# Kernel tuning notes

Measured on AMD Instinct MI355X. Metric: run time of the kernel, lower is better.

Reference implementation:

```python
import jax, jax.numpy as jnp
import numpy as np

N = 512
H = 128
L = 4
NUM_RBF = 50
CUTOFF = 5.0
NMOL = 16
OUT = 1


def setup_inputs() -> dict:
    key = jax.random.key(0)
    ks = jax.random.split(key, 12)
    s = lambda f: 1.0 / np.sqrt(f)
    atomic_numbers = jax.random.randint(ks[0], (N,), 0, 100)
    positions = jax.random.normal(ks[1], (N, 3), dtype=jnp.float32) * 2.0
    batch = jnp.sort(jax.random.randint(ks[2], (N,), 0, NMOL))
    return {
        'atomic_numbers': atomic_numbers,
        'positions': positions,
        'batch': batch,
        'embed': jax.random.normal(ks[3], (100, H), dtype=jnp.float32) * 0.1,
        'msg_w1': jax.random.normal(ks[4], (L, H + NUM_RBF + 3, H), dtype=jnp.float32) * s(H + NUM_RBF + 3),
        'msg_b1': jnp.zeros((L, H), jnp.float32),
        'msg_w2': jax.random.normal(ks[5], (L, H, H), dtype=jnp.float32) * s(H),
        'msg_b2': jnp.zeros((L, H), jnp.float32),
        'upd_w1': jax.random.normal(ks[6], (L, 2 * H, H), dtype=jnp.float32) * s(2 * H),
        'upd_b1': jnp.zeros((L, H), jnp.float32),
        'upd_w2': jax.random.normal(ks[7], (L, H, H), dtype=jnp.float32) * s(H),
        'upd_b2': jnp.zeros((L, H), jnp.float32),
        'out_w1': jax.random.normal(ks[8], (H, H // 2), dtype=jnp.float32) * s(H),
        'out_b1': jnp.zeros((H // 2,), jnp.float32),
        'out_w2': jax.random.normal(ks[9], (H // 2, OUT), dtype=jnp.float32) * s(H // 2),
        'out_b2': jnp.zeros((OUT,), jnp.float32),
    }


def _forward(atomic_numbers, positions, batch, embed, msg_w1, msg_b1, msg_w2,
             msg_b2, upd_w1, upd_b1, upd_w2, upd_b2, out_w1, out_b1, out_w2, out_b2):
    x = embed[jnp.clip(atomic_numbers, 0, 99)]                      # [N,H]
    # all-pairs geometry: row i = source, col j = target (matches repeat_interleave/repeat)
    diff = positions[:, None, :] - positions[None, :, :]            # [N,N,3]
    dist = jnp.linalg.norm(diff, axis=-1)                           # [N,N]
    not_self = jnp.arange(N)[:, None] != jnp.arange(N)[None, :]
    valid = (dist < CUTOFF) & not_self                              # [N,N] edge mask
    dirs = diff / jnp.maximum(dist, 1e-8)[..., None]                # [N,N,3]
    # gaussian RBF: centers linspace(0, cutoff, num_rbf), width = cutoff/num_rbf
    centers = jnp.linspace(0.0, CUTOFF, NUM_RBF)
    width = CUTOFF / NUM_RBF
    rbf = jnp.exp(-(dist[..., None] - centers) ** 2 / (2.0 * width ** 2))  # [N,N,50]

    for l in range(L):
        # Linear over concat([x_j, rbf, dirs]) split by input blocks (same math)
        Wx = msg_w1[l, :H]
        Wr = msg_w1[l, H:H + NUM_RBF]
        Wd = msg_w1[l, H + NUM_RBF:]
        pre = (x @ Wx)[:, None, :] \
            + jnp.einsum('ijr,rh->ijh', rbf, Wr) \
            + jnp.einsum('ijd,dh->ijh', dirs, Wd) + msg_b1[l]       # [N,N,H]
        m = jax.nn.silu(pre) @ msg_w2[l] + msg_b2[l]                # [N,N,H]
        m = jnp.where(valid[..., None], m, 0.0)
        aggr = m.sum(axis=0)                                        # scatter-add to target j
        upd_in = jnp.concatenate([x, aggr], axis=-1)                # [N,2H]
        x = x + jax.nn.silu(upd_in @ upd_w1[l] + upd_b1[l]) @ upd_w2[l] + upd_b2[l]

    # per-molecule mean pool
    sums = jax.ops.segment_sum(x, batch, num_segments=NMOL)         # [NMOL,H]
    counts = jax.ops.segment_sum(jnp.ones((N,), x.dtype), batch, num_segments=NMOL)
    pooled = sums / jnp.maximum(counts, 1.0)[:, None]
    return jax.nn.silu(pooled @ out_w1 + out_b1) @ out_w2 + out_b2  # [NMOL,OUT]


def reference(atomic_numbers, positions, batch, embed, msg_w1, msg_b1, msg_w2,
              msg_b2, upd_w1, upd_b1, upd_w2, upd_b2, out_w1, out_b1, out_w2, out_b2):
    return _forward(atomic_numbers, positions, batch, embed, msg_w1, msg_b1, msg_w2,
                    msg_b2, upd_w1, upd_b1, upd_w2, upd_b2, out_w1, out_b1, out_w2, out_b2)
```

## Files before the change

### kernel.cpp

```cpp
#include <hip/hip_runtime.h>
#include <math.h>

#define N 512
#define H 128
#define L 4
#define NUM_RBF 50
#define NMOL 16
#define SUPER 64
#define FSTRIDE 72

typedef __attribute__((ext_vector_type(8))) short short8;
typedef __attribute__((ext_vector_type(4))) float float4v;
typedef __attribute__((ext_vector_type(4))) int int4v;

__device__ __forceinline__ float silu_f(float v) {
    return v / (1.0f + __expf(-v));
}

__device__ __forceinline__ unsigned short f2bf(float f) {
    unsigned int u = __float_as_uint(f);
    unsigned int r = (u + 0x7FFFu + ((u >> 16) & 1u)) >> 16;
    return (unsigned short)r;
}

__global__ __launch_bounds__(512) void k_embed_lin(const int* __restrict__ an,
                                                   const float* __restrict__ embed,
                                                   const float* __restrict__ pos,
                                                   const float* __restrict__ wx,
                                                   const float* __restrict__ b1,
                                                   float* __restrict__ x,
                                                   float* __restrict__ a,
                                                   int* __restrict__ nbr,
                                                   int* __restrict__ ncnt) {
    int j = blockIdx.x;
    int tid = threadIdx.x;
    int lane = tid & 63;
    int wave = tid >> 6;
    int h = tid & 127;
    int grp = tid >> 7;

    __shared__ float xs[H];
    __shared__ int wsum8[8];
    __shared__ float part[4][H];

    float pjx = pos[j * 3 + 0], pjy = pos[j * 3 + 1], pjz = pos[j * 3 + 2];

    if (tid < H) {
        int z = an[j];
        z = min(max(z, 0), 99);
        float xv = embed[z * H + tid];
        xs[tid] = xv;
        x[j * H + tid] = xv;
    }

    {
        int i = tid;
        float dx = pos[i * 3 + 0] - pjx;
        float dy = pos[i * 3 + 1] - pjy;
        float dz = pos[i * 3 + 2] - pjz;
        float d2 = dx * dx + dy * dy + dz * dz;
        int valid = (d2 < 25.0f) && (i != j);
        unsigned long long m = __ballot(valid);
        int pre = __popcll(m & ((1ull << lane) - 1ull));
        if (lane == 0) wsum8[wave] = __popcll(m);
        __syncthreads();
        int wbase = 0, total = 0;
        for (int w = 0; w < 8; w++) {
            if (w < wave) wbase += wsum8[w];
            total += wsum8[w];
        }
        if (valid) nbr[j * 512 + wbase + pre] = i;
        int padded = (total + 63) & ~63;
        for (int s = total + tid; s < padded; s += 512) nbr[j * 512 + s] = j;
        if (tid == 0) ncnt[j] = total;
    }

    {
        float p0 = 0.f, p1 = 0.f, p2 = 0.f, p3 = 0.f;
        int k0 = grp * 32;
#pragma unroll 8
        for (int k = 0; k < 32; k += 4) {
            p0 += xs[k0 + k]     * wx[(k0 + k)     * H + h];
            p1 += xs[k0 + k + 1] * wx[(k0 + k + 1) * H + h];
            p2 += xs[k0 + k + 2] * wx[(k0 + k + 2) * H + h];
            p3 += xs[k0 + k + 3] * wx[(k0 + k + 3) * H + h];
        }
        part[grp][h] = (p0 + p1) + (p2 + p3);
    }
    __syncthreads();
    if (grp == 0)
        a[j * H + h] = part[0][h] + part[1][h] + part[2][h] + part[3][h] + b1[h];
}

__global__ __launch_bounds__(512) void k_layer(const float* __restrict__ a,
                                               const float* __restrict__ pos,
                                               const int* __restrict__ nbr,
                                               const int* __restrict__ ncnt,
                                               const float* __restrict__ wfeat,
                                               const float* __restrict__ w2,
                                               const float* __restrict__ b2,
                                               const float* __restrict__ u1,
                                               const float* __restrict__ ub1,
                                               const float* __restrict__ u2,
                                               const float* __restrict__ ub2,
                                               float* __restrict__ x,
                                               const float* __restrict__ wxn,
                                               const float* __restrict__ b1n,
                                               float* __restrict__ a_next) {
    int j = blockIdx.x;
    int tid = threadIdx.x;
    int g = tid >> 8;
    int t8 = tid & 255;
    int lane = tid & 63;
    int wv4 = (tid >> 6) & 3;
    int nn = lane & 15;
    int quad = lane >> 4;
    int hbase = wv4 * 32;

    __shared__ unsigned short F[2][2][SUPER * FSTRIDE];
    __shared__ int nidx[2][2][SUPER];
    __shared__ float sjp[2][H];
    __shared__ float sj[H], xj[H], ag[H], hid[H], xn[H];
    __shared__ float part[4][H];

    int cnt = ncnt[j];
    float pjx = pos[j * 3 + 0], pjy = pos[j * 3 + 1], pjz = pos[j * 3 + 2];

    if (tid < 2 * H) sjp[tid >> 7][tid & 127] = 0.0f;
    if (tid < H) xj[tid] = x[j * H + tid];

    short8 bfrag[2][2];
    for (int c = 0; c < 2; c++) {
        for (int t = 0; t < 2; t++) {
            short8 b;
            int h = hbase + 16 * t + nn;
#pragma unroll
            for (int jj = 0; jj < 8; jj++) {
                int k = c * 32 + quad * 8 + jj;
                float v = (k < NUM_RBF + 3) ? wfeat[k * H + h] : 0.0f;
                b[jj] = (short)f2bf(v);
            }
            bfrag[c][t] = b;
        }
    }

    const float DELTA = 5.0f / 49.0f;
    float pacc0 = 0.0f, pacc1 = 0.0f;

    int S = (cnt + 63) >> 6;
    int rounds = (S + 1) >> 1;

    int il = t8 >> 2;
    int kb = (t8 & 3) * 16;

    auto stage = [&](int s, int b) {
        int ni = nbr[j * 512 + s * 64 + il];
        if ((t8 & 3) == 0) nidx[g][b][il] = ni;
        float dx = pos[ni * 3 + 0] - pjx;
        float dy = pos[ni * 3 + 1] - pjy;
        float dz = pos[ni * 3 + 2] - pjz;
        float d = sqrtf(dx * dx + dy * dy + dz * dz);
        float rinv = 1.0f / fmaxf(d, 1e-8f);
        unsigned short vals[16];
#pragma unroll
        for (int qq = 0; qq < 16; qq++) {
            int k = kb + qq;
            float v;
            if (k < NUM_RBF) {
                float tt = d - (float)k * DELTA;
                v = __expf(-50.0f * tt * tt);
            } else if (k == NUM_RBF)     v = dx * rinv;
            else if (k == NUM_RBF + 1)   v = dy * rinv;
            else if (k == NUM_RBF + 2)   v = dz * rinv;
            else                         v = 0.0f;
            vals[qq] = f2bf(v);
        }
        unsigned int* dst = (unsigned int*)&F[g][b][il * FSTRIDE + kb];
#pragma unroll
        for (int qq = 0; qq < 8; qq++)
            dst[qq] = (unsigned int)vals[2 * qq] | ((unsigned int)vals[2 * qq + 1] << 16);
    };

    if (g < S) stage(g, 0);
    __syncthreads();

    for (int r = 0; r < rounds; r++) {
        int s = 2 * r + g;
        int sn = 2 * (r + 1) + g;
        if (sn < S) stage(sn, (r + 1) & 1);
        if (s < S) {
            int b = r & 1;
#pragma unroll
            for (int it = 0; it < SUPER / 16; it++) {
                int lbase = it * 16 + quad * 4;
                int4v ni4 = *(const int4v*)&nidx[g][b][lbase];
                float av0[4], av1[4];
#pragma unroll
                for (int rr = 0; rr < 4; rr++) {
                    av0[rr] = a[ni4[rr] * H + hbase + nn];
                    av1[rr] = a[ni4[rr] * H + hbase + 16 + nn];
                }
                short8 afrag0 = *(const short8*)&F[g][b][(it * 16 + nn) * FSTRIDE + 0 * 32 + quad * 8];
                short8 afrag1 = *(const short8*)&F[g][b][(it * 16 + nn) * FSTRIDE + 1 * 32 + quad * 8];
                float4v acc0 = {0.0f, 0.0f, 0.0f, 0.0f};
                float4v acc1 = {0.0f, 0.0f, 0.0f, 0.0f};
                acc0 = __builtin_amdgcn_mfma_f32_16x16x32_bf16(afrag0, bfrag[0][0], acc0, 0, 0, 0);
                acc0 = __builtin_amdgcn_mfma_f32_16x16x32_bf16(afrag1, bfrag[1][0], acc0, 0, 0, 0);
                acc1 = __builtin_amdgcn_mfma_f32_16x16x32_bf16(afrag0, bfrag[0][1], acc1, 0, 0, 0);
                acc1 = __builtin_amdgcn_mfma_f32_16x16x32_bf16(afrag1, bfrag[1][1], acc1, 0, 0, 0);
#pragma unroll
                for (int rr = 0; rr < 4; rr++) {
                    float vm = (s * 64 + lbase + rr < cnt) ? 1.0f : 0.0f;
                    pacc0 += vm * silu_f(acc0[rr] + av0[rr]);
                    pacc1 += vm * silu_f(acc1[rr] + av1[rr]);
                }
            }
        }
        __syncthreads();
    }

    pacc0 += __shfl_xor(pacc0, 16, 64);
    pacc0 += __shfl_xor(pacc0, 32, 64);
    pacc1 += __shfl_xor(pacc1, 16, 64);
    pacc1 += __shfl_xor(pacc1, 32, 64);
    if (lane < 16) {
        sjp[g][hbase + lane]      = pacc0;
        sjp[g][hbase + 16 + lane] = pacc1;
    }
    __syncthreads();
    if (tid < H) sj[tid] = sjp[0][tid] + sjp[1][tid];
    __syncthreads();

    int h = tid & 127;
    int grp = tid >> 7;

    {
        float p0 = 0.f, p1 = 0.f, p2 = 0.f, p3 = 0.f;
        int k0 = grp * 32;
#pragma unroll 8
        for (int k = 0; k < 32; k += 4) {
            p0 += sj[k0 + k]     * w2[(k0 + k)     * H + h];
            p1 += sj[k0 + k + 1] * w2[(k0 + k + 1) * H + h];
            p2 += sj[k0 + k + 2] * w2[(k0 + k + 2) * H + h];
            p3 += sj[k0 + k + 3] * w2[(k0 + k + 3) * H + h];
        }
        part[grp][h] = (p0 + p1) + (p2 + p3);
    }
    __syncthreads();
    if (grp == 0) ag[h] = part[0][h] + part[1][h] + part[2][h] + part[3][h] + (float)cnt * b2[h];
    __syncthreads();

    {
        const float* src = (grp < 2) ? xj : ag;
        int sbase = (grp & 1) * 64;
        int k0 = grp * 64;
        float p0 = 0.f, p1 = 0.f, p2 = 0.f, p3 = 0.f;
#pragma unroll 8
        for (int k = 0; k < 64; k += 4) {
            p0 += src[sbase + k]     * u1[(k0 + k)     * H + h];
            p1 += src[sbase + k + 1] * u1[(k0 + k + 1) * H + h];
            p2 += src[sbase + k + 2] * u1[(k0 + k + 2) * H + h];
            p3 += src[sbase + k + 3] * u1[(k0 + k + 3) * H + h];
        }
        part[grp][h] = (p0 + p1) + (p2 + p3);
    }
    __syncthreads();
    if (grp == 0) hid[h] = silu_f(part[0][h] + part[1][h] + part[2][h] + part[3][h] + ub1[h]);
    __syncthreads();

    {
        float p0 = 0.f, p1 = 0.f, p2 = 0.f, p3 = 0.f;
        int k0 = grp * 32;
#pragma unroll 8
        for (int k = 0; k < 32; k += 4) {
            p0 += hid[k0 + k]     * u2[(k0 + k)     * H + h];
            p1 += hid[k0 + k + 1] * u2[(k0 + k + 1) * H + h];
            p2 += hid[k0 + k + 2] * u2[(k0 + k + 2) * H + h];
            p3 += hid[k0 + k + 3] * u2[(k0 + k + 3) * H + h];
        }
        part[grp][h] = (p0 + p1) + (p2 + p3);
    }
    __syncthreads();
    if (grp == 0) {
        float xv = xj[h] + part[0][h] + part[1][h] + part[2][h] + part[3][h] + ub2[h];
        x[j * H + h] = xv;
        xn[h] = xv;
    }

    if (a_next != nullptr) {
        __syncthreads();
        float p0 = 0.f, p1 = 0.f, p2 = 0.f, p3 = 0.f;
        int k0 = grp * 32;
#pragma unroll 8
        for (int k = 0; k < 32; k += 4) {
            p0 += xn[k0 + k]     * wxn[(k0 + k)     * H + h];
            p1 += xn[k0 + k + 1] * wxn[(k0 + k + 1) * H + h];
            p2 += xn[k0 + k + 2] * wxn[(k0 + k + 2) * H + h];
            p3 += xn[k0 + k + 3] * wxn[(k0 + k + 3) * H + h];
        }
        part[grp][h] = (p0 + p1) + (p2 + p3);
        __syncthreads();
        if (grp == 0)
            a_next[j * H + h] = part[0][h] + part[1][h] + part[2][h] + part[3][h] + b1n[h];
    }
}

__global__ __launch_bounds__(H) void k_pool(const float* __restrict__ x,
                                            const int* __restrict__ batch,
                                            const float* __restrict__ ow1,
                                            const float* __restrict__ ob1,
                                            const float* __restrict__ ow2,
                                            const float* __restrict__ ob2,
                                            float* __restrict__ out) {
    int m = blockIdx.x;
    int h = threadIdx.x;
    __shared__ int lo_s, hi_s;
    __shared__ float pooled[H];
    __shared__ float hid[H / 2];

    if (h == 0) {
        int a = 0, b = N;
        while (a < b) { int mid = (a + b) >> 1; if (batch[mid] < m) a = mid + 1; else b = mid; }
        lo_s = a;
        b = N;
        while (a < b) { int mid = (a + b) >> 1; if (batch[mid] < m + 1) a = mid + 1; else b = mid; }
        hi_s = a;
    }
    __syncthreads();

    int lo = lo_s, hi = hi_s;
    float s = 0.0f;
    for (int i = lo; i < hi; i++) s += x[i * H + h];
    pooled[h] = s / (float)max(hi - lo, 1);
    __syncthreads();

    if (h < H / 2) {
        float p0 = 0.f, p1 = 0.f;
        for (int k = 0; k < H; k += 2) {
            p0 += pooled[k]     * ow1[(k)     * (H / 2) + h];
            p1 += pooled[k + 1] * ow1[(k + 1) * (H / 2) + h];
        }
        hid[h] = silu_f(p0 + p1 + ob1[h]);
    }
    __syncthreads();

    if (h == 0) {
        float o = ob2[0];
        for (int k = 0; k < H / 2; k++) o += hid[k] * ow2[k];
        out[m] = o;
    }
}

extern "C" void kernel_launch(void* const* d_in, const int* in_sizes, int n_in,
                              void* d_out, int out_size, void* d_ws, size_t ws_size,
                              hipStream_t stream) {
    const int*   an      = (const int*)d_in[0];
    const float* pos     = (const float*)d_in[1];
    const int*   batch   = (const int*)d_in[2];
    const float* embed   = (const float*)d_in[3];
    const float* msg_w1  = (const float*)d_in[4];
    const float* msg_b1  = (const float*)d_in[5];
    const float* msg_w2  = (const float*)d_in[6];
    const float* msg_b2  = (const float*)d_in[7];
    const float* upd_w1  = (const float*)d_in[8];
    const float* upd_b1  = (const float*)d_in[9];
    const float* upd_w2  = (const float*)d_in[10];
    const float* upd_b2  = (const float*)d_in[11];
    const float* out_w1  = (const float*)d_in[12];
    const float* out_b1  = (const float*)d_in[13];
    const float* out_w2  = (const float*)d_in[14];
    const float* out_b2  = (const float*)d_in[15];
    float* out = (float*)d_out;

    float* x    = (float*)d_ws;
    float* a0   = x + N * H;
    float* a1   = a0 + N * H;
    int*   nbr  = (int*)(a1 + N * H);
    int*   ncnt = nbr + N * 512;

    const int W1ROWS = H + NUM_RBF + 3;

    k_embed_lin<<<N, 512, 0, stream>>>(an, embed, pos, msg_w1, msg_b1, x, a0, nbr, ncnt);
    for (int l = 0; l < L; l++) {
        float* a_cur  = (l & 1) ? a1 : a0;
        float* a_next = (l + 1 < L) ? ((l & 1) ? a0 : a1) : nullptr;
        const float* wxn = (l + 1 < L) ? (msg_w1 + (l + 1) * W1ROWS * H) : nullptr;
        const float* b1n = (l + 1 < L) ? (msg_b1 + (l + 1) * H) : nullptr;
        k_layer<<<N, 512, 0, stream>>>(a_cur, pos, nbr, ncnt,
                                       msg_w1 + l * W1ROWS * H + H * H,
                                       msg_w2 + l * H * H, msg_b2 + l * H,
                                       upd_w1 + l * 2 * H * H, upd_b1 + l * H,
                                       upd_w2 + l * H * H, upd_b2 + l * H,
                                       x, wxn, b1n, a_next);
    }
    k_pool<<<NMOL, H, 0, stream>>>(x, batch, out_w1, out_b1, out_w2, out_b2, out);
}
```

Baseline: 221.7 us.

## Stage all neighbor feature tiles at once instead of double-buffered rounds

Replaces the per-group double-buffered stage/compute loop with a bulk phase. All 512 threads first build RBF/direction features for up to six 64-neighbor supertiles into a larger shared buffer, then both wave groups run the MFMA passes over them after a single barrier. This spreads feature generation across the whole block and removes the per-round barriers. In exchange it uses more LDS, which may lower occupancy, and it drops the overlap between staging and compute. The unused sjp zero-init is also removed.

```diff
diff --git a/kernel.cpp b/kernel.cpp
--- a/kernel.cpp
+++ b/kernel.cpp
@@ -8,6 +8,7 @@
 #define NMOL 16
 #define SUPER 64
 #define FSTRIDE 72
+#define SMAX 6
 
 typedef __attribute__((ext_vector_type(8))) short short8;
 typedef __attribute__((ext_vector_type(4))) float float4v;
@@ -110,15 +111,14 @@
     int j = blockIdx.x;
     int tid = threadIdx.x;
     int g = tid >> 8;
-    int t8 = tid & 255;
     int lane = tid & 63;
     int wv4 = (tid >> 6) & 3;
     int nn = lane & 15;
     int quad = lane >> 4;
     int hbase = wv4 * 32;
 
-    __shared__ unsigned short F[2][2][SUPER * FSTRIDE];
-    __shared__ int nidx[2][2][SUPER];
+    __shared__ unsigned short F[SMAX * SUPER * FSTRIDE];
+    __shared__ int nidx[SMAX * SUPER];
     __shared__ float sjp[2][H];
     __shared__ float sj[H], xj[H], ag[H], hid[H], xn[H];
     __shared__ float part[4][H];
@@ -126,7 +126,6 @@
     int cnt = ncnt[j];
     float pjx = pos[j * 3 + 0], pjy = pos[j * 3 + 1], pjz = pos[j * 3 + 2];
 
-    if (tid < 2 * H) sjp[tid >> 7][tid & 127] = 0.0f;
     if (tid < H) xj[tid] = x[j * H + tid];
 
     short8 bfrag[2][2];
@@ -148,60 +147,55 @@
     float pacc0 = 0.0f, pacc1 = 0.0f;
 
     int S = (cnt + 63) >> 6;
-    int rounds = (S + 1) >> 1;
-
-    int il = t8 >> 2;
-    int kb = (t8 & 3) * 16;
-
-    auto stage = [&](int s, int b) {
-        int ni = nbr[j * 512 + s * 64 + il];
-        if ((t8 & 3) == 0) nidx[g][b][il] = ni;
-        float dx = pos[ni * 3 + 0] - pjx;
-        float dy = pos[ni * 3 + 1] - pjy;
-        float dz = pos[ni * 3 + 2] - pjz;
-        float d = sqrtf(dx * dx + dy * dy + dz * dz);
-        float rinv = 1.0f / fmaxf(d, 1e-8f);
-        unsigned short vals[16];
-#pragma unroll
-        for (int qq = 0; qq < 16; qq++) {
-            int k = kb + qq;
-            float v;
-            if (k < NUM_RBF) {
-                float tt = d - (float)k * DELTA;
-                v = __expf(-50.0f * tt * tt);
-            } else if (k == NUM_RBF)     v = dx * rinv;
-            else if (k == NUM_RBF + 1)   v = dy * rinv;
-            else if (k == NUM_RBF + 2)   v = dz * rinv;
-            else                         v = 0.0f;
-            vals[qq] = f2bf(v);
-        }
-        unsigned int* dst = (unsigned int*)&F[g][b][il * FSTRIDE + kb];
-#pragma unroll
-        for (int qq = 0; qq < 8; qq++)
-            dst[qq] = (unsigned int)vals[2 * qq] | ((unsigned int)vals[2 * qq + 1] << 16);
+
+    auto stageAll = [&](int sbase, int S1) {
+        int totalStrips = S1 * SUPER * 4;
+        for (int strip = tid; strip < totalStrips; strip += 512) {
+            int row = strip >> 2;
+            int kb = (strip & 3) * 16;
+            int ni = nbr[j * 512 + sbase * SUPER + row];
+            if ((strip & 3) == 0) nidx[row] = ni;
+            float dx = pos[ni * 3 + 0] - pjx;
+            float dy = pos[ni * 3 + 1] - pjy;
+            float dz = pos[ni * 3 + 2] - pjz;
+            float d = sqrtf(dx * dx + dy * dy + dz * dz);
+            float rinv = 1.0f / fmaxf(d, 1e-8f);
+            unsigned short vals[16];
+#pragma unroll
+            for (int qq = 0; qq < 16; qq++) {
+                int k = kb + qq;
+                float v;
+                if (k < NUM_RBF) {
+                    float tt = d - (float)k * DELTA;
+                    v = __expf(-50.0f * tt * tt);
+                } else if (k == NUM_RBF)     v = dx * rinv;
+                else if (k == NUM_RBF + 1)   v = dy * rinv;
+                else if (k == NUM_RBF + 2)   v = dz * rinv;
+                else                         v = 0.0f;
+                vals[qq] = f2bf(v);
+            }
+            unsigned int* dst = (unsigned int*)&F[row * FSTRIDE + kb];
+#pragma unroll
+            for (int qq = 0; qq < 8; qq++)
+                dst[qq] = (unsigned int)vals[2 * qq] | ((unsigned int)vals[2 * qq + 1] << 16);
+        }
     };
 
-    if (g < S) stage(g, 0);
-    __syncthreads();
-
-    for (int r = 0; r < rounds; r++) {
-        int s = 2 * r + g;
-        int sn = 2 * (r + 1) + g;
-        if (sn < S) stage(sn, (r + 1) & 1);
-        if (s < S) {
-            int b = r & 1;
+    auto computeAll = [&](int sbase, int S1) {
+        for (int s = g; s < S1; s += 2) {
 #pragma unroll
             for (int it = 0; it < SUPER / 16; it++) {
-                int lbase = it * 16 + quad * 4;
-                int4v ni4 = *(const int4v*)&nidx[g][b][lbase];
+                int lrow = s * SUPER + it * 16;
+                int lbase = lrow + quad * 4;
+                int4v ni4 = *(const int4v*)&nidx[lbase];
                 float av0[4], av1[4];
 #pragma unroll
                 for (int rr = 0; rr < 4; rr++) {
                     av0[rr] = a[ni4[rr] * H + hbase + nn];
                     av1[rr] = a[ni4[rr] * H + hbase + 16 + nn];
                 }
-                short8 afrag0 = *(const short8*)&F[g][b][(it * 16 + nn) * FSTRIDE + 0 * 32 + quad * 8];
-                short8 afrag1 = *(const short8*)&F[g][b][(it * 16 + nn) * FSTRIDE + 1 * 32 + quad * 8];
+                short8 afrag0 = *(const short8*)&F[(lrow + nn) * FSTRIDE + 0 * 32 + quad * 8];
+                short8 afrag1 = *(const short8*)&F[(lrow + nn) * FSTRIDE + 1 * 32 + quad * 8];
                 float4v acc0 = {0.0f, 0.0f, 0.0f, 0.0f};
                 float4v acc1 = {0.0f, 0.0f, 0.0f, 0.0f};
                 acc0 = __builtin_amdgcn_mfma_f32_16x16x32_bf16(afrag0, bfrag[0][0], acc0, 0, 0, 0);
@@ -210,13 +204,24 @@
                 acc1 = __builtin_amdgcn_mfma_f32_16x16x32_bf16(afrag1, bfrag[1][1], acc1, 0, 0, 0);
 #pragma unroll
                 for (int rr = 0; rr < 4; rr++) {
-                    float vm = (s * 64 + lbase + rr < cnt) ? 1.0f : 0.0f;
+                    float vm = ((sbase + s) * SUPER + it * 16 + quad * 4 + rr < cnt) ? 1.0f : 0.0f;
                     pacc0 += vm * silu_f(acc0[rr] + av0[rr]);
                     pacc1 += vm * silu_f(acc1[rr] + av1[rr]);
                 }
             }
         }
+    };
+
+    int S0 = min(S, SMAX);
+    stageAll(0, S0);
+    __syncthreads();
+    computeAll(0, S0);
+    for (int sb = SMAX; sb < S; sb += SMAX) {
+        int S1 = min(S - sb, SMAX);
         __syncthreads();
+        stageAll(sb, S1);
+        __syncthreads();
+        computeAll(sb, S1);
     }
 
     pacc0 += __shfl_xor(pacc0, 16, 64);
```

Result: slower. 231.0 us (+4.2%).
